# Kernel optimization log

Hardware: AMD Instinct MI355X
Metric: run time of the kernel (lower is better)

## Reference

```python
import jax, jax.numpy as jnp
import numpy as np

N = 100000   # nodes
E = 1000000  # edges
DS = 16      # stage start/end scale-out vec dim
DC = 224     # raw context dim
CC = DS + DC + DS  # context_channels = 256
DM = 128     # stage_metrics_channels
H = (CC + DM) // 2  # 192 hidden of final_transform
OUT = 128    # out_channels (== DM, required by overwrite path)


def setup_inputs() -> dict:
    key = jax.random.key(0)
    ks = jax.random.split(key, 16)
    n = lambda k, shape, s=0.05: jax.random.normal(k, shape, jnp.float32) * s
    return {
        "edge_index": jax.random.randint(ks[0], (2, E), 0, N, dtype=jnp.int64),
        "stage_start": jax.random.normal(ks[1], (N, DS), jnp.float32),
        "stage_end": jax.random.normal(ks[2], (N, DS), jnp.float32),
        "context": jax.random.normal(ks[3], (N, DC), jnp.float32),
        "stage_metrics": jax.random.normal(ks[4], (N, DM), jnp.float32),
        "W_l": n(ks[5], (CC, CC)), "b_l": jnp.zeros((CC,), jnp.float32),
        "W_r": n(ks[6], (CC, CC)), "b_r": jnp.zeros((CC,), jnp.float32),
        "att": n(ks[7], (CC,)),
        "W1": n(ks[8], (CC + DM, H)), "b1": jnp.zeros((H,), jnp.float32),
        "W2": n(ks[9], (H, OUT)), "b2": jnp.zeros((OUT,), jnp.float32),
        "bias": jnp.zeros((OUT,), jnp.float32),
    }


def reference(edge_index, stage_start, stage_end, context, stage_metrics,
              W_l, b_l, W_r, b_r, att, W1, b1, W2, b2, bias):
    # node transform: [N, CC]
    nc = jnp.concatenate([stage_start, context, stage_end], axis=-1)
    cl = nc @ W_l + b_l  # source-side (j)
    cr = nc @ W_r + b_r  # target-side (i)

    src, dst = edge_index[0], edge_index[1]  # flow: source_to_target, aggregate by dst
    ci = cr[dst]                 # [E, CC] context_i
    cj = cl[src]                 # [E, CC] context_j
    mj = stage_metrics[src]      # [E, DM] metrics_j

    ctx = jax.nn.selu(ci + cj)
    ctx = jnp.where(jnp.all(mj == 0, axis=1, keepdims=True), 0.0, ctx)

    alpha = ctx @ att            # [E]
    mask = alpha != 0            # ~zero_indices

    # segment softmax over non-zero alphas, grouped by dst (PyG softmax: sub max, exp, /sum+eps)
    NEG = jnp.float32(-1e30)
    m = jax.ops.segment_max(jnp.where(mask, alpha, NEG), dst, num_segments=N)
    ex = jnp.where(mask, jnp.exp(alpha - m[dst]), 0.0)
    s = jax.ops.segment_sum(ex, dst, num_segments=N)
    a = jnp.where(mask, ex / (s[dst] + 1e-16), 0.0)

    # per-edge 2-layer SELU MLP
    h = jax.nn.selu(jnp.concatenate([ctx, mj], axis=-1) @ W1 + b1)  # [E, H]
    f = jax.nn.selu(h @ W2 + b2)                                    # [E, OUT]
    msg = jnp.where(mask[:, None], f * a[:, None], 0.0)

    # scatter-add aggregation to nodes
    out = jax.ops.segment_sum(msg, dst, num_segments=N)  # [N, OUT]

    # rows with all-zero aggregation are overwritten by stage_metrics; others get bias + sigmoid
    ovr = jnp.all(out == 0, axis=1, keepdims=True)
    return jnp.where(ovr, stage_metrics, jax.nn.sigmoid(out + bias))
```

## Files before the change

### kernel.cpp

```cpp
#include <hip/hip_runtime.h>
#include <hip/hip_bf16.h>
#include <math.h>

#define NN   100000
#define EE   1000000
#define CCH  256
#define DMC  128
#define HDC  192
#define OUTC 128
#define ET   64
#define MS   132
#define GS   391

typedef unsigned short u16;
using bf16x8 = __attribute__((ext_vector_type(8))) short;
using f32x4  = __attribute__((ext_vector_type(4))) float;
using u16x4  = __attribute__((ext_vector_type(4))) unsigned short;
using u16x8  = __attribute__((ext_vector_type(8))) unsigned short;

__device__ __forceinline__ float selu_f(float x) {
    const float sc = 1.0507009873554804934193349852946f;
    const float c1 = 1.7580993408473765792727863477367f;
    const float e = __expf(x);
    return x > 0.0f ? sc * x : __builtin_fmaf(c1, e, -c1);
}
__device__ __forceinline__ u16 f2bf(float f) {
    union { __hip_bfloat16 h; u16 u; } c;
    c.h = __float2bfloat16(f);
    return c.u;
}
__device__ __forceinline__ float bf2f(u16 h) {
    return __uint_as_float(((unsigned int)h) << 16);
}

__global__ __launch_bounds__(256, 2) void k_node_gemm(
    const float* __restrict__ ss, const float* __restrict__ se,
    const float* __restrict__ ctx, const u16* __restrict__ W0p,
    const float* __restrict__ bl, const float* __restrict__ br,
    u16* __restrict__ clb, u16* __restrict__ crb)
{
    __shared__ __align__(16) char Xs[64 * 512];
    const int tid = threadIdx.x;
    const int wave = tid >> 6, lane = tid & 63;
    const int node0 = blockIdx.x * 64;

    {
        const int r = lane;
        const int nd = min(node0 + r, NN - 1);
#pragma unroll
        for (int i = 0; i < 8; ++i) {
            const int c0 = wave * 64 + i * 8;
            float4 va, vb;
            {
                const int c = c0;
                if (c < 16)       va = *reinterpret_cast<const float4*>(ss + nd * 16 + c);
                else if (c < 240) va = *reinterpret_cast<const float4*>(ctx + (size_t)nd * 224 + (c - 16));
                else              va = *reinterpret_cast<const float4*>(se + nd * 16 + (c - 240));
            }
            {
                const int c = c0 + 4;
                if (c < 16)       vb = *reinterpret_cast<const float4*>(ss + nd * 16 + c);
                else if (c < 240) vb = *reinterpret_cast<const float4*>(ctx + (size_t)nd * 224 + (c - 16));
                else              vb = *reinterpret_cast<const float4*>(se + nd * 16 + (c - 240));
            }
            u16x8 v;
            v[0] = f2bf(va.x); v[1] = f2bf(va.y); v[2] = f2bf(va.z); v[3] = f2bf(va.w);
            v[4] = f2bf(vb.x); v[5] = f2bf(vb.y); v[6] = f2bf(vb.z); v[7] = f2bf(vb.w);
            *reinterpret_cast<u16x8*>(Xs + r * 512 + ((c0 * 2) ^ ((r & 7) << 4))) = v;
        }
    }
    __syncthreads();

    const int r16   = lane & 15;
    const int khalf = (lane >> 4) << 4;
    const int rbase = (lane >> 4) * 4;

    f32x4 acc[4][8];
#pragma unroll
    for (int m = 0; m < 4; ++m)
#pragma unroll
        for (int jj = 0; jj < 8; ++jj) acc[m][jj] = (f32x4){0.f, 0.f, 0.f, 0.f};

    for (int ks = 0; ks < 8; ++ks) {
        bf16x8 b[8];
#pragma unroll
        for (int jj = 0; jj < 8; ++jj)
            b[jj] = *reinterpret_cast<const bf16x8*>(
                W0p + (((size_t)(wave + 4 * jj) * 8 + ks) * 64 + lane) * 8);
        const int kb = ks * 64 + khalf;
#pragma unroll
        for (int m = 0; m < 4; ++m) {
            const int row = m * 16 + r16;
            const bf16x8 a = *reinterpret_cast<const bf16x8*>(
                Xs + row * 512 + (kb ^ ((row & 7) << 4)));
#pragma unroll
            for (int jj = 0; jj < 8; ++jj)
                acc[m][jj] = __builtin_amdgcn_mfma_f32_16x16x32_bf16(a, b[jj], acc[m][jj], 0, 0, 0);
        }
    }

#pragma unroll
    for (int jj = 0; jj < 8; ++jj) {
        const int nt = wave + 4 * jj;
        const bool isL = nt < 16;
        const int ncl = (isL ? nt * 16 : (nt - 16) * 16) + r16;
        const float bias = isL ? bl[ncl] : br[ncl];
        u16* base = (isL ? clb : crb) + ncl;
#pragma unroll
        for (int m = 0; m < 4; ++m)
#pragma unroll
            for (int rr = 0; rr < 4; ++rr) {
                const int node = node0 + m * 16 + rbase + rr;
                if (node < NN)
                    base[(size_t)node * CCH] = f2bf(acc[m][jj][rr] + bias);
            }
    }
}

__global__ __launch_bounds__(256) void k_convert(
    const float* __restrict__ in, u16* __restrict__ out, int n)
{
    const int i = (blockIdx.x * 256 + threadIdx.x) * 4;
    if (i < n) {
        const float4 v = *reinterpret_cast<const float4*>(in + i);
        u16x4 o; o[0] = f2bf(v.x); o[1] = f2bf(v.y); o[2] = f2bf(v.z); o[3] = f2bf(v.w);
        *reinterpret_cast<u16x4*>(out + i) = o;
    }
}

__device__ __forceinline__ void pack_frag(
    const float* __restrict__ W, u16* __restrict__ out, int K, int N,
    int f, int lane)
{
    const int KS = K >> 5;
    const int nt = f / KS, ks = f - nt * KS;
    const int n = nt * 16 + (lane & 15);
    const int k0 = ks * 32 + (lane >> 4) * 8;
    u16x8 v;
#pragma unroll
    for (int j = 0; j < 8; ++j) v[j] = f2bf(W[(size_t)(k0 + j) * N + n]);
    *reinterpret_cast<u16x8*>(out + ((size_t)f * 64 + lane) * 8) = v;
}

__global__ __launch_bounds__(64) void k_pack_all(
    const float* __restrict__ Wl, const float* __restrict__ Wr,
    const float* __restrict__ W1, const float* __restrict__ W2,
    const float* __restrict__ att,
    u16* __restrict__ W0p, u16* __restrict__ W1p, u16* __restrict__ W2p,
    u16* __restrict__ attp)
{
    const int b = blockIdx.x, lane = threadIdx.x;
    if (b < 128)       pack_frag(Wl, W0p, CCH, CCH, b, lane);
    else if (b < 256)  pack_frag(Wr, W0p + (size_t)128 * 64 * 8, CCH, CCH, b - 128, lane);
    else if (b < 400)  pack_frag(W1, W1p, CCH + DMC, HDC, b - 256, lane);
    else if (b < 448)  pack_frag(W2, W2p, HDC, OUTC, b - 400, lane);
    else {
        const int ks = b - 448;
        const int nloc = lane & 15;
        const int k0 = ks * 32 + (lane >> 4) * 8;
        u16x8 v;
#pragma unroll
        for (int j = 0; j < 8; ++j) v[j] = f2bf((nloc == 0) ? att[k0 + j] : 0.f);
        *reinterpret_cast<u16x8*>(attp + ((size_t)ks * 64 + lane) * 8) = v;
    }
}

__global__ __launch_bounds__(256) void k_hist(
    const int* __restrict__ ei, int* __restrict__ cnt)
{
    const int i = blockIdx.x * 256 + threadIdx.x;
    if (i < EE / 4) {
        const int4 d = *reinterpret_cast<const int4*>(ei + EE + i * 4);
        atomicAdd(&cnt[d.x], 1); atomicAdd(&cnt[d.y], 1);
        atomicAdd(&cnt[d.z], 1); atomicAdd(&cnt[d.w], 1);
    }
}

__global__ __launch_bounds__(256) void k_scan1(
    const int* __restrict__ cnt, int* __restrict__ bsum)
{
    const int i = blockIdx.x * 256 + threadIdx.x;
    int v = (i < NN) ? cnt[i] : 0;
#pragma unroll
    for (int o = 1; o < 64; o <<= 1) v += __shfl_xor(v, o);
    __shared__ int ws[4];
    if ((threadIdx.x & 63) == 0) ws[threadIdx.x >> 6] = v;
    __syncthreads();
    if (threadIdx.x == 0) bsum[blockIdx.x] = ws[0] + ws[1] + ws[2] + ws[3];
}

__global__ __launch_bounds__(512) void k_scan2(int* __restrict__ bsum)
{
    __shared__ int s[512];
    const int t = threadIdx.x;
    const int v = (t < GS) ? bsum[t] : 0;
    s[t] = v;
    __syncthreads();
    for (int o = 1; o < 512; o <<= 1) {
        const int u = (t >= o) ? s[t - o] : 0;
        __syncthreads();
        s[t] += u;
        __syncthreads();
    }
    if (t < GS) bsum[t] = s[t] - v;
}

__global__ __launch_bounds__(256) void k_scan3(
    const int* __restrict__ cnt, const int* __restrict__ bsum,
    int* __restrict__ cur)
{
    const int t = threadIdx.x;
    const int i = blockIdx.x * 256 + t;
    const int lane = t & 63, w = t >> 6;
    const int v = (i < NN) ? cnt[i] : 0;
    int x = v;
#pragma unroll
    for (int o = 1; o < 64; o <<= 1) {
        const int u = __shfl_up(x, o);
        if (lane >= o) x += u;
    }
    __shared__ int wsum[4];
    if (lane == 63) wsum[w] = x;
    __syncthreads();
    int off = bsum[blockIdx.x];
    for (int k2 = 0; k2 < w; ++k2) off += wsum[k2];
    if (i < NN) cur[i] = off + x - v;
}

__global__ __launch_bounds__(256) void k_scatter(
    const int* __restrict__ ei, int* __restrict__ cur, int2* __restrict__ sd)
{
    const int i = blockIdx.x * 256 + threadIdx.x;
    if (i < EE) {
        const int d = ei[EE + i];
        const int pos = atomicAdd(&cur[d], 1);
        sd[pos] = make_int2(ei[i], d);
    }
}

__global__ __launch_bounds__(512, 6) void k_edge_mlp(
    const int2* __restrict__ sd,
    const u16* __restrict__ clb, const u16* __restrict__ crb,
    const u16* __restrict__ metb, const u16* __restrict__ attp,
    float* __restrict__ sb,
    const u16* __restrict__ W1p, const float* __restrict__ b1,
    const u16* __restrict__ W2p, const float* __restrict__ b2,
    float* __restrict__ dout)
{
    __shared__ __align__(16) char Xs[ET * 768];
    __shared__ int esrc[ET], edst[ET], flg[ET];
    __shared__ float exs[ET];

    const int tid  = threadIdx.x;
    const int wave = tid >> 6;
    const int lane = tid & 63;
    const int wm = wave >> 2, wn = wave & 3;
    const int ebase = blockIdx.x * ET;

    if (tid < ET) {
        const int2 p = sd[ebase + tid];
        esrc[tid] = p.x;
        edst[tid] = p.y;
    }
    __syncthreads();

    u16x8 rv[4], lv[4], mv[2];
#pragma unroll
    for (int i = 0; i < 4; ++i) {
        const int k = tid + i * 512;
        const int t = k >> 5, c = k & 31;
        rv[i] = *reinterpret_cast<const u16x8*>(crb + (size_t)edst[t] * CCH + c * 8);
        lv[i] = *reinterpret_cast<const u16x8*>(clb + (size_t)esrc[t] * CCH + c * 8);
    }
#pragma unroll
    for (int i = 0; i < 2; ++i) {
        const int k = tid + i * 512;
        mv[i] = *reinterpret_cast<const u16x8*>(metb + (size_t)esrc[k >> 4] * DMC + (k & 15) * 8);
    }
#pragma unroll
    for (int i = 0; i < 4; ++i) {
        const int k = tid + i * 512;
        const int t = k >> 5, c = k & 31;
        u16x8 v;
#pragma unroll
        for (int j = 0; j < 8; ++j) v[j] = f2bf(selu_f(bf2f(rv[i][j]) + bf2f(lv[i][j])));
        *reinterpret_cast<u16x8*>(Xs + t * 768 + ((c * 16) ^ ((t & 7) << 4))) = v;
    }
#pragma unroll
    for (int i = 0; i < 2; ++i) {
        const int k = tid + i * 512;
        const int t = k >> 4, g = k & 15;
        unsigned ob = 0;
#pragma unroll
        for (int j = 0; j < 8; ++j) ob |= (unsigned)mv[i][j];
        const bool nz = (ob & 0x7fffu) != 0u;
        const unsigned long long bal = __ballot(nz);
        if ((lane & 15) == 0)
            flg[t] = (int)((bal >> ((lane >> 4) * 16)) & 0xFFFFull) != 0;
        *reinterpret_cast<u16x8*>(Xs + t * 768 + (((32 + g) * 16) ^ ((t & 7) << 4))) = mv[i];
    }
    __syncthreads();

    const int r16   = lane & 15;
    const int khalf = (lane >> 4) << 4;
    const int rbase = (lane >> 4) * 4;

    f32x4 acc[2][3];
    f32x4 acc3[2];
#pragma unroll
    for (int m = 0; m < 2; ++m) {
#pragma unroll
        for (int j = 0; j < 3; ++j) acc[m][j] = (f32x4){0.f, 0.f, 0.f, 0.f};
        acc3[m] = (f32x4){0.f, 0.f, 0.f, 0.f};
    }

    for (int ks = 0; ks < 12; ++ks) {
        bf16x8 b[3];
#pragma unroll
        for (int j = 0; j < 3; ++j)
            b[j] = *reinterpret_cast<const bf16x8*>(
                W1p + (((size_t)(wn + 4 * j) * 12 + ks) * 64 + lane) * 8);
        bf16x8 b3 = {};
        const bool doA = (wn == 0) && (ks < 8);
        if (doA)
            b3 = *reinterpret_cast<const bf16x8*>(attp + ((size_t)ks * 64 + lane) * 8);
        const int kb = ks * 64 + khalf;
#pragma unroll
        for (int m = 0; m < 2; ++m) {
            const int row = (wm * 2 + m) * 16 + r16;
            const bf16x8 a = *reinterpret_cast<const bf16x8*>(
                Xs + row * 768 + (kb ^ ((row & 7) << 4)));
#pragma unroll
            for (int j = 0; j < 3; ++j)
                acc[m][j] = __builtin_amdgcn_mfma_f32_16x16x32_bf16(a, b[j], acc[m][j], 0, 0, 0);
            if (doA)
                acc3[m] = __builtin_amdgcn_mfma_f32_16x16x32_bf16(a, b3, acc3[m], 0, 0, 0);
        }
    }

    if (wn == 0 && r16 == 0) {
        const int hi = lane >> 4;
#pragma unroll
        for (int m = 0; m < 2; ++m)
#pragma unroll
            for (int r = 0; r < 4; ++r) {
                const int e = (wm * 2 + m) * 16 + hi * 4 + r;
                const float al = acc3[m][r];
                exs[e] = (flg[e] && al != 0.f) ? __expf(al) : 0.f;
            }
    }
    __syncthreads();

#pragma unroll
    for (int j = 0; j < 3; ++j) {
        const int n = (wn + 4 * j) * 16 + r16;
        const float bb = b1[n];
#pragma unroll
        for (int m = 0; m < 2; ++m)
#pragma unroll
            for (int r = 0; r < 4; ++r) {
                const int row = (wm * 2 + m) * 16 + rbase + r;
                *reinterpret_cast<u16*>(Xs + row * 384 + ((n * 2) ^ ((row & 7) << 4))) =
                    f2bf(selu_f(acc[m][j][r] + bb));
            }
    }
    __syncthreads();

    f32x4 acc2[2][2];
#pragma unroll
    for (int m = 0; m < 2; ++m)
#pragma unroll
        for (int j = 0; j < 2; ++j) acc2[m][j] = (f32x4){0.f, 0.f, 0.f, 0.f};

    for (int ks = 0; ks < 6; ++ks) {
        bf16x8 b[2];
#pragma unroll
        for (int j = 0; j < 2; ++j)
            b[j] = *reinterpret_cast<const bf16x8*>(
                W2p + (((size_t)(wn + 4 * j) * 6 + ks) * 64 + lane) * 8);
        const int kb = ks * 64 + khalf;
#pragma unroll
        for (int m = 0; m < 2; ++m) {
            const int row = (wm * 2 + m) * 16 + r16;
            const bf16x8 a = *reinterpret_cast<const bf16x8*>(
                Xs + row * 384 + (kb ^ ((row & 7) << 4)));
#pragma unroll
            for (int j = 0; j < 2; ++j)
                acc2[m][j] = __builtin_amdgcn_mfma_f32_16x16x32_bf16(a, b[j], acc2[m][j], 0, 0, 0);
        }
    }
    __syncthreads();

    float* Ms = (float*)Xs;
#pragma unroll
    for (int j = 0; j < 2; ++j) {
        const int n = (wn + 4 * j) * 16 + r16;
        const float bb = b2[n];
#pragma unroll
        for (int m = 0; m < 2; ++m)
#pragma unroll
            for (int r = 0; r < 4; ++r) {
                const int e = (wm * 2 + m) * 16 + rbase + r;
                Ms[e * MS + n] = selu_f(acc2[m][j][r] + bb) * exs[e];
            }
    }
    if (tid < ET) Ms[tid * MS + 128] = exs[tid];
    __syncthreads();

    {
        const int col = tid & 127;
        const int h = tid >> 7;
        const int r0 = h * 16;
        int cur_d = edst[r0];
        float s = Ms[r0 * MS + col];
        for (int r = r0 + 1; r < r0 + 16; ++r) {
            const int d = edst[r];
            const float v = Ms[r * MS + col];
            if (d != cur_d) {
                if (s != 0.f) atomicAdd(&dout[(size_t)cur_d * OUTC + col], s);
                cur_d = d; s = v;
            } else {
                s += v;
            }
        }
        if (s != 0.f) atomicAdd(&dout[(size_t)cur_d * OUTC + col], s);
    }
    if (tid < 4) {
        const int r0 = tid * 16;
        int cur_d = edst[r0];
        float s = Ms[r0 * MS + 128];
        for (int r = r0 + 1; r < r0 + 16; ++r) {
            const int d = edst[r];
            const float v = Ms[r * MS + 128];
            if (d != cur_d) {
                if (s != 0.f) atomicAdd(&sb[cur_d], s);
                cur_d = d; s = v;
            } else {
                s += v;
            }
        }
        if (s != 0.f) atomicAdd(&sb[cur_d], s);
    }
}

__global__ __launch_bounds__(256) void k_finalize(
    float* __restrict__ dout, const float* __restrict__ met,
    const float* __restrict__ bias, const float* __restrict__ sb)
{
    const int n = blockIdx.x * 4 + (threadIdx.x >> 6);
    const int lane = threadIdx.x & 63;
    const float a0 = dout[(size_t)n * OUTC + lane];
    const float a1 = dout[(size_t)n * OUTC + 64 + lane];
    const bool ovr = __all((a0 == 0.f) && (a1 == 0.f));
    float r0, r1;
    if (ovr) {
        r0 = met[(size_t)n * DMC + lane];
        r1 = met[(size_t)n * DMC + 64 + lane];
    } else {
        const float inv = 1.0f / (sb[n] + 1e-16f);
        r0 = 1.f / (1.f + __expf(-(a0 * inv + bias[lane])));
        r1 = 1.f / (1.f + __expf(-(a1 * inv + bias[64 + lane])));
    }
    dout[(size_t)n * OUTC + lane] = r0;
    dout[(size_t)n * OUTC + 64 + lane] = r1;
}

extern "C" void kernel_launch(void* const* d_in, const int* in_sizes, int n_in,
                              void* d_out, int out_size, void* d_ws, size_t ws_size,
                              hipStream_t stream)
{
    const int*   ei   = (const int*)d_in[0];
    const float* ss   = (const float*)d_in[1];
    const float* se   = (const float*)d_in[2];
    const float* ctx  = (const float*)d_in[3];
    const float* met  = (const float*)d_in[4];
    const float* Wl   = (const float*)d_in[5];
    const float* bl   = (const float*)d_in[6];
    const float* Wr   = (const float*)d_in[7];
    const float* br   = (const float*)d_in[8];
    const float* att  = (const float*)d_in[9];
    const float* W1   = (const float*)d_in[10];
    const float* b1   = (const float*)d_in[11];
    const float* W2   = (const float*)d_in[12];
    const float* b2   = (const float*)d_in[13];
    const float* bias = (const float*)d_in[14];

    u16* clb  = (u16*)d_ws;
    u16* crb  = clb  + (size_t)NN * CCH;
    u16* metb = crb  + (size_t)NN * CCH;
    u16* W1p  = metb + (size_t)NN * DMC;
    u16* W2p  = W1p  + (size_t)(CCH + DMC) * HDC;
    u16* W0p  = W2p  + (size_t)HDC * OUTC;
    float* sb = (float*)(W0p + (size_t)CCH * 512);
    int* cnt  = (int*)(sb + NN);
    int* cur  = cnt + NN;
    int2* sd  = (int2*)(cur + NN);
    int* bsum = (int*)(sd + EE);
    u16* attp = (u16*)(bsum + 512);

    float* dout = (float*)d_out;

    hipMemsetAsync(dout, 0, (size_t)NN * OUTC * sizeof(float), stream);
    hipMemsetAsync(sb, 0, (size_t)NN * 2 * sizeof(float), stream);

    k_hist<<<(EE / 4 + 255) / 256, 256, 0, stream>>>(ei, cnt);
    k_scan1<<<GS, 256, 0, stream>>>(cnt, bsum);
    k_scan2<<<1, 512, 0, stream>>>(bsum);
    k_scan3<<<GS, 256, 0, stream>>>(cnt, bsum, cur);
    k_scatter<<<(EE + 255) / 256, 256, 0, stream>>>(ei, cur, sd);

    k_pack_all<<<456, 64, 0, stream>>>(Wl, Wr, W1, W2, att, W0p, W1p, W2p, attp);
    k_convert<<<(NN * DMC / 4 + 255) / 256, 256, 0, stream>>>(met, metb, NN * DMC);

    k_node_gemm<<<(NN + 63) / 64, 256, 0, stream>>>(ss, se, ctx, W0p, bl, br, clb, crb);
    k_edge_mlp<<<EE / ET, 512, 0, stream>>>(sd, clb, crb, metb, attp, sb,
                                            W1p, b1, W2p, b2, dout);
    k_finalize<<<NN / 4, 256, 0, stream>>>(dout, met, bias, sb);
}
```

Measured before the change: 681.5 us.

## Halve edge-MLP LDS footprint by splitting K into two staged halves

The shared X tile is cut from 768 to 384 bytes per edge. The first GEMM's K dimension is processed in two phases: gather and SELU the first 192 context channels, run 6 k-steps, then reload the remaining context plus metrics into the same buffer and run the last 6. The per-edge message staging buffer also moves from fp32 to bf16, and launch bounds go from 6 to 8 waves-per-SIMD to allow more resident blocks. This adds an extra barrier phase and a second gather stage, and rounds the messages to bf16 before the atomic adds, which may lose accuracy.

```diff
diff --git a/kernel.cpp b/kernel.cpp
--- a/kernel.cpp
+++ b/kernel.cpp
@@ -9,7 +9,7 @@
 #define HDC  192
 #define OUTC 128
 #define ET   64
-#define MS   132
+#define MSB  132
 #define GS   391
 
 typedef unsigned short u16;
@@ -238,7 +238,7 @@
     }
 }
 
-__global__ __launch_bounds__(512, 6) void k_edge_mlp(
+__global__ __launch_bounds__(512, 8) void k_edge_mlp(
     const int2* __restrict__ sd,
     const u16* __restrict__ clb, const u16* __restrict__ crb,
     const u16* __restrict__ metb, const u16* __restrict__ attp,
@@ -247,7 +247,7 @@
     const u16* __restrict__ W2p, const float* __restrict__ b2,
     float* __restrict__ dout)
 {
-    __shared__ __align__(16) char Xs[ET * 768];
+    __shared__ __align__(16) char Xs[ET * 384];
     __shared__ int esrc[ET], edst[ET], flg[ET];
     __shared__ float exs[ET];
 
@@ -264,57 +264,91 @@
     }
     __syncthreads();
 
-    u16x8 rv[4], lv[4], mv[2];
-#pragma unroll
-    for (int i = 0; i < 4; ++i) {
-        const int k = tid + i * 512;
-        const int t = k >> 5, c = k & 31;
-        rv[i] = *reinterpret_cast<const u16x8*>(crb + (size_t)edst[t] * CCH + c * 8);
-        lv[i] = *reinterpret_cast<const u16x8*>(clb + (size_t)esrc[t] * CCH + c * 8);
-    }
-#pragma unroll
-    for (int i = 0; i < 2; ++i) {
-        const int k = tid + i * 512;
-        mv[i] = *reinterpret_cast<const u16x8*>(metb + (size_t)esrc[k >> 4] * DMC + (k & 15) * 8);
-    }
-#pragma unroll
-    for (int i = 0; i < 4; ++i) {
-        const int k = tid + i * 512;
-        const int t = k >> 5, c = k & 31;
-        u16x8 v;
-#pragma unroll
-        for (int j = 0; j < 8; ++j) v[j] = f2bf(selu_f(bf2f(rv[i][j]) + bf2f(lv[i][j])));
-        *reinterpret_cast<u16x8*>(Xs + t * 768 + ((c * 16) ^ ((t & 7) << 4))) = v;
-    }
-#pragma unroll
-    for (int i = 0; i < 2; ++i) {
-        const int k = tid + i * 512;
-        const int t = k >> 4, g = k & 15;
+    const int t  = tid >> 3;
+    const int b8 = tid & 7;
+    const int tswz = (t & 7) << 4;
+
+    {
+        const u16* cr = crb + (size_t)edst[t] * CCH;
+        const u16* cl = clb + (size_t)esrc[t] * CCH;
+        u16x8 rA[3], lA[3];
+#pragma unroll
+        for (int i = 0; i < 3; ++i) {
+            const int g = b8 + i * 8;
+            rA[i] = *reinterpret_cast<const u16x8*>(cr + g * 8);
+            lA[i] = *reinterpret_cast<const u16x8*>(cl + g * 8);
+        }
+#pragma unroll
+        for (int i = 0; i < 3; ++i) {
+            const int g = b8 + i * 8;
+            u16x8 v;
+#pragma unroll
+            for (int j = 0; j < 8; ++j) v[j] = f2bf(selu_f(bf2f(rA[i][j]) + bf2f(lA[i][j])));
+            *reinterpret_cast<u16x8*>(Xs + t * 384 + ((g * 16) ^ tswz)) = v;
+        }
+    }
+    __syncthreads();
+
+    const int r16   = lane & 15;
+    const int khalf = (lane >> 4) << 4;
+    const int rb4   = (lane >> 4) * 4;
+
+    f32x4 acc[2][3];
+    f32x4 acc3[2];
+#pragma unroll
+    for (int m = 0; m < 2; ++m) {
+#pragma unroll
+        for (int j = 0; j < 3; ++j) acc[m][j] = (f32x4){0.f, 0.f, 0.f, 0.f};
+        acc3[m] = (f32x4){0.f, 0.f, 0.f, 0.f};
+    }
+
+    for (int ks = 0; ks < 6; ++ks) {
+        bf16x8 b[3];
+#pragma unroll
+        for (int j = 0; j < 3; ++j)
+            b[j] = *reinterpret_cast<const bf16x8*>(
+                W1p + (((size_t)(wn + 4 * j) * 12 + ks) * 64 + lane) * 8);
+        bf16x8 b3 = {};
+        const bool doA = (wn == 0);
+        if (doA)
+            b3 = *reinterpret_cast<const bf16x8*>(attp + ((size_t)ks * 64 + lane) * 8);
+        const int kb = ks * 64 + khalf;
+#pragma unroll
+        for (int m = 0; m < 2; ++m) {
+            const int row = (wm * 2 + m) * 16 + r16;
+            const bf16x8 a = *reinterpret_cast<const bf16x8*>(
+                Xs + row * 384 + (kb ^ ((row & 7) << 4)));
+#pragma unroll
+            for (int j = 0; j < 3; ++j)
+                acc[m][j] = __builtin_amdgcn_mfma_f32_16x16x32_bf16(a, b[j], acc[m][j], 0, 0, 0);
+            if (doA)
+                acc3[m] = __builtin_amdgcn_mfma_f32_16x16x32_bf16(a, b3, acc3[m], 0, 0, 0);
+        }
+    }
+    __syncthreads();
+
+    {
+        const u16x8 rB = *reinterpret_cast<const u16x8*>(crb + (size_t)edst[t] * CCH + (24 + b8) * 8);
+        const u16x8 lB = *reinterpret_cast<const u16x8*>(clb + (size_t)esrc[t] * CCH + (24 + b8) * 8);
+        const u16x8 m0 = *reinterpret_cast<const u16x8*>(metb + (size_t)esrc[t] * DMC + b8 * 8);
+        const u16x8 m1 = *reinterpret_cast<const u16x8*>(metb + (size_t)esrc[t] * DMC + (b8 + 8) * 8);
         unsigned ob = 0;
 #pragma unroll
-        for (int j = 0; j < 8; ++j) ob |= (unsigned)mv[i][j];
+        for (int j = 0; j < 8; ++j) ob |= (unsigned)m0[j] | (unsigned)m1[j];
         const bool nz = (ob & 0x7fffu) != 0u;
         const unsigned long long bal = __ballot(nz);
-        if ((lane & 15) == 0)
-            flg[t] = (int)((bal >> ((lane >> 4) * 16)) & 0xFFFFull) != 0;
-        *reinterpret_cast<u16x8*>(Xs + t * 768 + (((32 + g) * 16) ^ ((t & 7) << 4))) = mv[i];
-    }
-    __syncthreads();
-
-    const int r16   = lane & 15;
-    const int khalf = (lane >> 4) << 4;
-    const int rbase = (lane >> 4) * 4;
-
-    f32x4 acc[2][3];
-    f32x4 acc3[2];
-#pragma unroll
-    for (int m = 0; m < 2; ++m) {
-#pragma unroll
-        for (int j = 0; j < 3; ++j) acc[m][j] = (f32x4){0.f, 0.f, 0.f, 0.f};
-        acc3[m] = (f32x4){0.f, 0.f, 0.f, 0.f};
-    }
-
-    for (int ks = 0; ks < 12; ++ks) {
+        if ((lane & 7) == 0)
+            flg[t] = ((bal >> (lane & 56)) & 0xFFull) != 0;
+        u16x8 v;
+#pragma unroll
+        for (int j = 0; j < 8; ++j) v[j] = f2bf(selu_f(bf2f(rB[j]) + bf2f(lB[j])));
+        *reinterpret_cast<u16x8*>(Xs + t * 384 + ((b8 * 16) ^ tswz)) = v;
+        *reinterpret_cast<u16x8*>(Xs + t * 384 + (((8 + b8) * 16) ^ tswz)) = m0;
+        *reinterpret_cast<u16x8*>(Xs + t * 384 + (((16 + b8) * 16) ^ tswz)) = m1;
+    }
+    __syncthreads();
+
+    for (int ks = 6; ks < 12; ++ks) {
         bf16x8 b[3];
 #pragma unroll
         for (int j = 0; j < 3; ++j)
@@ -324,12 +358,12 @@
         const bool doA = (wn == 0) && (ks < 8);
         if (doA)
             b3 = *reinterpret_cast<const bf16x8*>(attp + ((size_t)ks * 64 + lane) * 8);
-        const int kb = ks * 64 + khalf;
+        const int kb = (ks - 6) * 64 + khalf;
 #pragma unroll
         for (int m = 0; m < 2; ++m) {
             const int row = (wm * 2 + m) * 16 + r16;
             const bf16x8 a = *reinterpret_cast<const bf16x8*>(
-                Xs + row * 768 + (kb ^ ((row & 7) << 4)));
+                Xs + row * 384 + (kb ^ ((row & 7) << 4)));
 #pragma unroll
             for (int j = 0; j < 3; ++j)
                 acc[m][j] = __builtin_amdgcn_mfma_f32_16x16x32_bf16(a, b[j], acc[m][j], 0, 0, 0);
@@ -359,7 +393,7 @@
         for (int m = 0; m < 2; ++m)
 #pragma unroll
             for (int r = 0; r < 4; ++r) {
-                const int row = (wm * 2 + m) * 16 + rbase + r;
+                const int row = (wm * 2 + m) * 16 + rb4 + r;
                 *reinterpret_cast<u16*>(Xs + row * 384 + ((n * 2) ^ ((row & 7) << 4))) =
                     f2bf(selu_f(acc[m][j][r] + bb));
             }
@@ -391,7 +425,7 @@
     }
     __syncthreads();
 
-    float* Ms = (float*)Xs;
+    u16* Ms = (u16*)Xs;
 #pragma unroll
     for (int j = 0; j < 2; ++j) {
         const int n = (wn + 4 * j) * 16 + r16;
@@ -400,11 +434,10 @@
         for (int m = 0; m < 2; ++m)
 #pragma unroll
             for (int r = 0; r < 4; ++r) {
-                const int e = (wm * 2 + m) * 16 + rbase + r;
-                Ms[e * MS + n] = selu_f(acc2[m][j][r] + bb) * exs[e];
-            }
-    }
-    if (tid < ET) Ms[tid * MS + 128] = exs[tid];
+                const int e = (wm * 2 + m) * 16 + rb4 + r;
+                Ms[e * MSB + n] = f2bf(selu_f(acc2[m][j][r] + bb) * exs[e]);
+            }
+    }
     __syncthreads();
 
     {
@@ -412,10 +445,10 @@
         const int h = tid >> 7;
         const int r0 = h * 16;
         int cur_d = edst[r0];
-        float s = Ms[r0 * MS + col];
+        float s = bf2f(Ms[r0 * MSB + col]);
         for (int r = r0 + 1; r < r0 + 16; ++r) {
             const int d = edst[r];
-            const float v = Ms[r * MS + col];
+            const float v = bf2f(Ms[r * MSB + col]);
             if (d != cur_d) {
                 if (s != 0.f) atomicAdd(&dout[(size_t)cur_d * OUTC + col], s);
                 cur_d = d; s = v;
@@ -428,10 +461,10 @@
     if (tid < 4) {
         const int r0 = tid * 16;
         int cur_d = edst[r0];
-        float s = Ms[r0 * MS + 128];
+        float s = exs[r0];
         for (int r = r0 + 1; r < r0 + 16; ++r) {
             const int d = edst[r];
-            const float v = Ms[r * MS + 128];
+            const float v = exs[r];
             if (d != cur_d) {
                 if (s != 0.f) atomicAdd(&sb[cur_d], s);
                 cur_d = d; s = v;
```

Result: slower. 869.1 us (+27.5%).

## Use 1024-thread edge blocks with shrunk LDS and bf16 message staging

Applied to the files above, without the earlier changes.

The edge MLP kernel now runs 1024 threads per block, so each wave owns one 16-row M tile instead of two. The first GEMM is split into a context phase and a metrics phase so the X tile fits in 512 bytes per row, with the metrics loaded after the context K-steps. The per-edge messages are staged in LDS as bf16 instead of fp32, and the softmax denominators are read straight from exs. The aim is less LDS per block and fewer registers per thread, giving more resident waves to hide gather latency, at the cost of extra barriers and bf16 rounding of the messages before the atomics.

```diff
diff --git a/kernel.cpp b/kernel.cpp
--- a/kernel.cpp
+++ b/kernel.cpp
@@ -9,7 +9,7 @@
 #define HDC  192
 #define OUTC 128
 #define ET   64
-#define MS   132
+#define MSB  132
 #define GS   391
 
 typedef unsigned short u16;
@@ -238,7 +238,7 @@
     }
 }
 
-__global__ __launch_bounds__(512, 6) void k_edge_mlp(
+__global__ __launch_bounds__(1024, 8) void k_edge_mlp(
     const int2* __restrict__ sd,
     const u16* __restrict__ clb, const u16* __restrict__ crb,
     const u16* __restrict__ metb, const u16* __restrict__ attp,
@@ -247,7 +247,7 @@
     const u16* __restrict__ W2p, const float* __restrict__ b2,
     float* __restrict__ dout)
 {
-    __shared__ __align__(16) char Xs[ET * 768];
+    __shared__ __align__(16) char Xs[ET * 512];
     __shared__ int esrc[ET], edst[ET], flg[ET];
     __shared__ float exs[ET];
 
@@ -264,90 +264,85 @@
     }
     __syncthreads();
 
-    u16x8 rv[4], lv[4], mv[2];
-#pragma unroll
-    for (int i = 0; i < 4; ++i) {
-        const int k = tid + i * 512;
+#pragma unroll
+    for (int i = 0; i < 2; ++i) {
+        const int k = tid + i * 1024;
         const int t = k >> 5, c = k & 31;
-        rv[i] = *reinterpret_cast<const u16x8*>(crb + (size_t)edst[t] * CCH + c * 8);
-        lv[i] = *reinterpret_cast<const u16x8*>(clb + (size_t)esrc[t] * CCH + c * 8);
-    }
-#pragma unroll
-    for (int i = 0; i < 2; ++i) {
-        const int k = tid + i * 512;
-        mv[i] = *reinterpret_cast<const u16x8*>(metb + (size_t)esrc[k >> 4] * DMC + (k & 15) * 8);
-    }
-#pragma unroll
-    for (int i = 0; i < 4; ++i) {
-        const int k = tid + i * 512;
-        const int t = k >> 5, c = k & 31;
+        const u16x8 r = *reinterpret_cast<const u16x8*>(crb + (size_t)edst[t] * CCH + c * 8);
+        const u16x8 l = *reinterpret_cast<const u16x8*>(clb + (size_t)esrc[t] * CCH + c * 8);
         u16x8 v;
 #pragma unroll
-        for (int j = 0; j < 8; ++j) v[j] = f2bf(selu_f(bf2f(rv[i][j]) + bf2f(lv[i][j])));
-        *reinterpret_cast<u16x8*>(Xs + t * 768 + ((c * 16) ^ ((t & 7) << 4))) = v;
-    }
-#pragma unroll
-    for (int i = 0; i < 2; ++i) {
-        const int k = tid + i * 512;
-        const int t = k >> 4, g = k & 15;
+        for (int j = 0; j < 8; ++j) v[j] = f2bf(selu_f(bf2f(r[j]) + bf2f(l[j])));
+        *reinterpret_cast<u16x8*>(Xs + t * 512 + ((c * 16) ^ ((t & 7) << 4))) = v;
+    }
+    __syncthreads();
+
+    const int r16   = lane & 15;
+    const int khalf = (lane >> 4) << 4;
+    const int rb4   = (lane >> 4) * 4;
+
+    f32x4 acc[3];
+    f32x4 acc3;
+#pragma unroll
+    for (int j = 0; j < 3; ++j) acc[j] = (f32x4){0.f, 0.f, 0.f, 0.f};
+    acc3 = (f32x4){0.f, 0.f, 0.f, 0.f};
+
+    for (int ks = 0; ks < 8; ++ks) {
+        bf16x8 b[3];
+#pragma unroll
+        for (int j = 0; j < 3; ++j)
+            b[j] = *reinterpret_cast<const bf16x8*>(
+                W1p + (((size_t)(wn + 4 * j) * 12 + ks) * 64 + lane) * 8);
+        bf16x8 b3 = {};
+        if (wn == 0)
+            b3 = *reinterpret_cast<const bf16x8*>(attp + ((size_t)ks * 64 + lane) * 8);
+        const int row = wm * 16 + r16;
+        const bf16x8 a = *reinterpret_cast<const bf16x8*>(
+            Xs + row * 512 + ((ks * 64 + khalf) ^ ((row & 7) << 4)));
+#pragma unroll
+        for (int j = 0; j < 3; ++j)
+            acc[j] = __builtin_amdgcn_mfma_f32_16x16x32_bf16(a, b[j], acc[j], 0, 0, 0);
+        if (wn == 0)
+            acc3 = __builtin_amdgcn_mfma_f32_16x16x32_bf16(a, b3, acc3, 0, 0, 0);
+    }
+    __syncthreads();
+
+    {
+        const int t = tid >> 4, g = tid & 15;
+        const u16x8 m = *reinterpret_cast<const u16x8*>(metb + (size_t)esrc[t] * DMC + g * 8);
         unsigned ob = 0;
 #pragma unroll
-        for (int j = 0; j < 8; ++j) ob |= (unsigned)mv[i][j];
+        for (int j = 0; j < 8; ++j) ob |= (unsigned)m[j];
         const bool nz = (ob & 0x7fffu) != 0u;
         const unsigned long long bal = __ballot(nz);
         if ((lane & 15) == 0)
             flg[t] = (int)((bal >> ((lane >> 4) * 16)) & 0xFFFFull) != 0;
-        *reinterpret_cast<u16x8*>(Xs + t * 768 + (((32 + g) * 16) ^ ((t & 7) << 4))) = mv[i];
-    }
-    __syncthreads();
-
-    const int r16   = lane & 15;
-    const int khalf = (lane >> 4) << 4;
-    const int rbase = (lane >> 4) * 4;
-
-    f32x4 acc[2][3];
-    f32x4 acc3[2];
-#pragma unroll
-    for (int m = 0; m < 2; ++m) {
-#pragma unroll
-        for (int j = 0; j < 3; ++j) acc[m][j] = (f32x4){0.f, 0.f, 0.f, 0.f};
-        acc3[m] = (f32x4){0.f, 0.f, 0.f, 0.f};
-    }
-
-    for (int ks = 0; ks < 12; ++ks) {
+        *reinterpret_cast<u16x8*>(Xs + t * 512 + ((g * 16) ^ ((t & 7) << 4))) = m;
+    }
+    __syncthreads();
+
+    if (wn == 0 && r16 == 0) {
+        const int hi = lane >> 4;
+#pragma unroll
+        for (int r = 0; r < 4; ++r) {
+            const int e = wm * 16 + hi * 4 + r;
+            const float al = acc3[r];
+            exs[e] = (flg[e] && al != 0.f) ? __expf(al) : 0.f;
+        }
+    }
+
+    for (int ks = 8; ks < 12; ++ks) {
         bf16x8 b[3];
 #pragma unroll
         for (int j = 0; j < 3; ++j)
             b[j] = *reinterpret_cast<const bf16x8*>(
                 W1p + (((size_t)(wn + 4 * j) * 12 + ks) * 64 + lane) * 8);
-        bf16x8 b3 = {};
-        const bool doA = (wn == 0) && (ks < 8);
-        if (doA)
-            b3 = *reinterpret_cast<const bf16x8*>(attp + ((size_t)ks * 64 + lane) * 8);
-        const int kb = ks * 64 + khalf;
-#pragma unroll
-        for (int m = 0; m < 2; ++m) {
-            const int row = (wm * 2 + m) * 16 + r16;
-            const bf16x8 a = *reinterpret_cast<const bf16x8*>(
-                Xs + row * 768 + (kb ^ ((row & 7) << 4)));
-#pragma unroll
-            for (int j = 0; j < 3; ++j)
-                acc[m][j] = __builtin_amdgcn_mfma_f32_16x16x32_bf16(a, b[j], acc[m][j], 0, 0, 0);
-            if (doA)
-                acc3[m] = __builtin_amdgcn_mfma_f32_16x16x32_bf16(a, b3, acc3[m], 0, 0, 0);
-        }
-    }
-
-    if (wn == 0 && r16 == 0) {
-        const int hi = lane >> 4;
-#pragma unroll
-        for (int m = 0; m < 2; ++m)
-#pragma unroll
-            for (int r = 0; r < 4; ++r) {
-                const int e = (wm * 2 + m) * 16 + hi * 4 + r;
-                const float al = acc3[m][r];
-                exs[e] = (flg[e] && al != 0.f) ? __expf(al) : 0.f;
-            }
+        const int row = wm * 16 + r16;
+        const bf16x8 a = *reinterpret_cast<const bf16x8*>(
+            Xs + row * 512 + (((ks - 8) * 64 + khalf) ^ ((row & 7) << 4)));
+#pragma unroll
+        for (int j = 0; j < 3; ++j)
+            acc[j] = __builtin_amdgcn_mfma_f32_16x16x32_bf16(a, b[j], acc[j], 0, 0, 0);
     }
     __syncthreads();
 
@@ -356,21 +351,17 @@
         const int n = (wn + 4 * j) * 16 + r16;
         const float bb = b1[n];
 #pragma unroll
-        for (int m = 0; m < 2; ++m)
-#pragma unroll
-            for (int r = 0; r < 4; ++r) {
-                const int row = (wm * 2 + m) * 16 + rbase + r;
-                *reinterpret_cast<u16*>(Xs + row * 384 + ((n * 2) ^ ((row & 7) << 4))) =
-                    f2bf(selu_f(acc[m][j][r] + bb));
-            }
-    }
-    __syncthreads();
-
-    f32x4 acc2[2][2];
-#pragma unroll
-    for (int m = 0; m < 2; ++m)
-#pragma unroll
-        for (int j = 0; j < 2; ++j) acc2[m][j] = (f32x4){0.f, 0.f, 0.f, 0.f};
+        for (int r = 0; r < 4; ++r) {
+            const int row = wm * 16 + rb4 + r;
+            *reinterpret_cast<u16*>(Xs + row * 512 + ((n * 2) ^ ((row & 7) << 4))) =
+                f2bf(selu_f(acc[j][r] + bb));
+        }
+    }
+    __syncthreads();
+
+    f32x4 acc2[2];
+#pragma unroll
+    for (int j = 0; j < 2; ++j) acc2[j] = (f32x4){0.f, 0.f, 0.f, 0.f};
 
     for (int ks = 0; ks < 6; ++ks) {
         bf16x8 b[2];
@@ -378,44 +369,37 @@
         for (int j = 0; j < 2; ++j)
             b[j] = *reinterpret_cast<const bf16x8*>(
                 W2p + (((size_t)(wn + 4 * j) * 6 + ks) * 64 + lane) * 8);
-        const int kb = ks * 64 + khalf;
-#pragma unroll
-        for (int m = 0; m < 2; ++m) {
-            const int row = (wm * 2 + m) * 16 + r16;
-            const bf16x8 a = *reinterpret_cast<const bf16x8*>(
-                Xs + row * 384 + (kb ^ ((row & 7) << 4)));
-#pragma unroll
-            for (int j = 0; j < 2; ++j)
-                acc2[m][j] = __builtin_amdgcn_mfma_f32_16x16x32_bf16(a, b[j], acc2[m][j], 0, 0, 0);
-        }
-    }
-    __syncthreads();
-
-    float* Ms = (float*)Xs;
+        const int row = wm * 16 + r16;
+        const bf16x8 a = *reinterpret_cast<const bf16x8*>(
+            Xs + row * 512 + ((ks * 64 + khalf) ^ ((row & 7) << 4)));
+#pragma unroll
+        for (int j = 0; j < 2; ++j)
+            acc2[j] = __builtin_amdgcn_mfma_f32_16x16x32_bf16(a, b[j], acc2[j], 0, 0, 0);
+    }
+    __syncthreads();
+
+    u16* Ms = (u16*)Xs;
 #pragma unroll
     for (int j = 0; j < 2; ++j) {
         const int n = (wn + 4 * j) * 16 + r16;
         const float bb = b2[n];
 #pragma unroll
-        for (int m = 0; m < 2; ++m)
-#pragma unroll
-            for (int r = 0; r < 4; ++r) {
-                const int e = (wm * 2 + m) * 16 + rbase + r;
-                Ms[e * MS + n] = selu_f(acc2[m][j][r] + bb) * exs[e];
-            }
-    }
-    if (tid < ET) Ms[tid * MS + 128] = exs[tid];
+        for (int r = 0; r < 4; ++r) {
+            const int e = wm * 16 + rb4 + r;
+            Ms[e * MSB + n] = f2bf(selu_f(acc2[j][r] + bb) * exs[e]);
+        }
+    }
     __syncthreads();
 
     {
         const int col = tid & 127;
         const int h = tid >> 7;
-        const int r0 = h * 16;
+        const int r0 = h * 8;
         int cur_d = edst[r0];
-        float s = Ms[r0 * MS + col];
-        for (int r = r0 + 1; r < r0 + 16; ++r) {
+        float s = bf2f(Ms[r0 * MSB + col]);
+        for (int r = r0 + 1; r < r0 + 8; ++r) {
             const int d = edst[r];
-            const float v = Ms[r * MS + col];
+            const float v = bf2f(Ms[r * MSB + col]);
             if (d != cur_d) {
                 if (s != 0.f) atomicAdd(&dout[(size_t)cur_d * OUTC + col], s);
                 cur_d = d; s = v;
@@ -425,13 +409,13 @@
         }
         if (s != 0.f) atomicAdd(&dout[(size_t)cur_d * OUTC + col], s);
     }
-    if (tid < 4) {
-        const int r0 = tid * 16;
+    if (tid < 8) {
+        const int r0 = tid * 8;
         int cur_d = edst[r0];
-        float s = Ms[r0 * MS + 128];
-        for (int r = r0 + 1; r < r0 + 16; ++r) {
+        float s = exs[r0];
+        for (int r = r0 + 1; r < r0 + 8; ++r) {
             const int d = edst[r];
-            const float v = Ms[r * MS + 128];
+            const float v = exs[r];
             if (d != cur_d) {
                 if (s != 0.f) atomicAdd(&sb[cur_d], s);
                 cur_d = d; s = v;
@@ -513,7 +497,7 @@
     k_convert<<<(NN * DMC / 4 + 255) / 256, 256, 0, stream>>>(met, metb, NN * DMC);
 
     k_node_gemm<<<(NN + 63) / 64, 256, 0, stream>>>(ss, se, ctx, W0p, bl, br, clb, crb);
-    k_edge_mlp<<<EE / ET, 512, 0, stream>>>(sd, clb, crb, metb, attp, sb,
-                                            W1p, b1, W2p, b2, dout);
+    k_edge_mlp<<<EE / ET, 1024, 0, stream>>>(sd, clb, crb, metb, attp, sb,
+                                             W1p, b1, W2p, b2, dout);
     k_finalize<<<NN / 4, 256, 0, stream>>>(dout, met, bias, sb);
 }
```

Measured after the change: 872.4 us. +28.0%, slower.
